# Kernel tuning notes

Hardware: AMD Instinct MI355X
Metric: run time of the kernel (lower is better)

Reference implementation:

```python
import jax, jax.numpy as jnp
import numpy as np

TOL = 1e-3


def _image_grads(F):
    # replicate-pad central difference, matches GradientBatch (conv with [-0.5,0,0.5])
    Fx = jnp.pad(F, ((0, 0), (0, 0), (0, 0), (1, 1)), mode='edge')
    gx = 0.5 * (Fx[:, :, :, 2:] - Fx[:, :, :, :-2])
    Fy = jnp.pad(F, ((0, 0), (0, 0), (1, 1), (0, 0)), mode='edge')
    gy = 0.5 * (Fy[:, :, 2:, :] - Fy[:, :, :-2, :])
    return gx, gy


def _param_to_H(p):
    B = p.shape[0]
    z = jnp.zeros((B, 1, 1), p.dtype)
    return jnp.concatenate([p, z], 1).reshape(B, 3, 3) + jnp.eye(3, dtype=p.dtype)


def _bilinear_sample(A, xw, yw):
    # grid_sample(mode='bilinear', align_corners=True, padding_mode='zeros') at pixel coords (xw, yw)
    B, k, h, w = A.shape
    x0 = jnp.floor(xw)
    y0 = jnp.floor(yw)
    fx = (xw - x0).reshape(B, 1, h * w)
    fy = (yw - y0).reshape(B, 1, h * w)
    Af = A.reshape(B, k, h * w)

    def gather(xi, yi):
        valid = (xi >= 0) & (xi <= w - 1) & (yi >= 0) & (yi <= h - 1)
        xi_c = jnp.clip(xi, 0, w - 1).astype(jnp.int32)
        yi_c = jnp.clip(yi, 0, h - 1).astype(jnp.int32)
        idx = (yi_c * w + xi_c).reshape(B, 1, h * w)
        v = jnp.take_along_axis(Af, jnp.broadcast_to(idx, (B, k, h * w)), axis=2)
        return v * valid.reshape(B, 1, h * w).astype(A.dtype)

    v00 = gather(x0, y0)
    v01 = gather(x0 + 1, y0)
    v10 = gather(x0, y0 + 1)
    v11 = gather(x0 + 1, y0 + 1)
    Q = ((1 - fx) * (1 - fy) * v00 + fx * (1 - fy) * v01
         + (1 - fx) * fy * v10 + fx * fy * v11)
    return Q.reshape(B, k, h, w)


def _deeplk(img, temp, init_param, max_itr):
    B, k, h, w = temp.shape
    dt = temp.dtype
    gx, gy = _image_grads(temp)
    # centered pixel grid (meshgrid in source: x - x.max()/2)
    x = jnp.arange(w, dtype=dt) - (w - 1) / 2.0
    y = jnp.arange(h, dtype=dt) - (h - 1) / 2.0
    X, Y = jnp.meshgrid(x, y)  # (h, w); X varies along w
    Xf = jnp.tile(X.reshape(-1), k)  # [k*h*w], tiled per channel
    Yf = jnp.tile(Y.reshape(-1), k)
    gxf = gx.reshape(B, k * h * w)
    gyf = gy.reshape(B, k * h * w)
    dIdp = jnp.stack([
        Xf * gxf, Yf * gxf, gxf,
        Xf * gyf, Yf * gyf, gyf,
        -Xf * Xf * gxf - Xf * Yf * gyf,
        -Xf * Yf * gxf - Yf * Yf * gyf,
    ], axis=2)  # [B, k*h*w, 8]
    Hmat = jnp.einsum('bnp,bnq->bpq', dIdp, dIdp)  # [B,8,8]
    invH = jnp.linalg.inv(Hmat)
    invH_dIdp = jnp.einsum('bpq,bnq->bpn', invH, dIdp)  # [B,8,k*h*w]
    xy = jnp.stack([X.reshape(-1), Y.reshape(-1), jnp.ones((h * w,), dt)], 0)  # [3, h*w]
    tolf = jnp.asarray(TOL, dt)

    def step(carry, _):
        p, dp = carry
        Hm = _param_to_H(p)
        xyw = jnp.einsum('bij,jn->bin', Hm, xy)  # [B,3,h*w]
        Xw = (xyw[:, 0] / xyw[:, 2]).reshape(B, h, w) + (w - 1) / 2.0
        Yw = (xyw[:, 1] / xyw[:, 2]).reshape(B, h, w) + (h - 1) / 2.0
        Fi_warp = _bilinear_sample(img, Xw, Yw)
        xn = Xw / ((w - 1) / 2.0) - 1.0
        yn = Yw / ((h - 1) / 2.0) - 1.0
        mask = ((xn > -1 + 2.0 / w) & (xn < 1 - 2.0 / w)
                & (yn > -1 + 2.0 / h) & (yn < 1 - 2.0 / h)).astype(dt)
        r = (Fi_warp - temp * mask[:, None]).reshape(B, k * h * w, 1)
        dp_new = jnp.einsum('bpn,bnj->bpj', invH_dIdp, r)  # [B,8,1]
        dp_new = dp_new.at[:, 6:8, 0].set(0.0)  # zero projective terms
        active = (jnp.linalg.norm(dp, axis=1, keepdims=True) > tolf).astype(dt)
        dp2 = active * dp_new  # converged samples freeze (dp stays 0)
        return (p - dp2, dp2), None

    dp0 = jnp.ones((B, 8, 1), dt)
    (p, _), _ = jax.lax.scan(step, (init_param, dp0), None, length=max_itr)
    return p


def setup_inputs() -> dict:
    key = jax.random.key(0)
    k1, k2 = jax.random.split(key)
    B, k, h, w = 8, 8, 256, 256
    img = jax.random.normal(k1, (B, k, h, w), dtype=jnp.float32)
    temp = jax.random.normal(k2, (B, k, h, w), dtype=jnp.float32)
    init_param = jnp.zeros((B, 8, 1), dtype=jnp.float32)
    return {"img": img, "temp": temp, "init_param": init_param, "max_itr": 10}


def reference(img, temp, init_param, max_itr):
    p = _deeplk(img, temp, init_param, max_itr)
    return (p, _param_to_H(p))
```

## Files before the change

kernel.cpp:

```cpp
#include <hip/hip_runtime.h>
#include <hip/hip_bf16.h>

#define B_ 8
#define K_ 8
#define H_ 256
#define W_ 256
#define HW (H_*W_)

__device__ __forceinline__ unsigned short f2bf(float f) {
    __hip_bfloat16 h = __float2bfloat16(f);
    return *reinterpret_cast<unsigned short*>(&h);
}
__device__ __forceinline__ void ub8(uint4 u, float* o) {
    o[0] = __uint_as_float(u.x << 16); o[1] = __uint_as_float(u.x & 0xffff0000u);
    o[2] = __uint_as_float(u.y << 16); o[3] = __uint_as_float(u.y & 0xffff0000u);
    o[4] = __uint_as_float(u.z << 16); o[5] = __uint_as_float(u.z & 0xffff0000u);
    o[6] = __uint_as_float(u.w << 16); o[7] = __uint_as_float(u.w & 0xffff0000u);
}
__device__ __forceinline__ float half_reduce(float v) {
    v += __shfl_down(v, 16, 64);
    v += __shfl_down(v, 8, 64);
    v += __shfl_down(v, 4, 64);
    v += __shfl_down(v, 2, 64);
    v += __shfl_down(v, 1, 64);
    return v;
}

__device__ __forceinline__ void pixel_accum(
    const uint4* __restrict__ imgT, const uint4* __restrict__ TG,
    int b, int x, int y,
    float h00, float h01, float h02, float h10, float h11, float h12,
    float h20, float h21, float* aa) {
    const int px = (y << 8) | x;
    const float X = (float)x - 127.5f, Y = (float)y - 127.5f;
    const float zw = h20 * X + h21 * Y + 1.f;
    const float Xw = (h00 * X + h01 * Y + h02) / zw + 127.5f;
    const float Yw = (h10 * X + h11 * Y + h12) / zw + 127.5f;
    const float NLO = -1.f + 2.f / 256.f, NHI = 1.f - 2.f / 256.f;
    const float xn = Xw / 127.5f - 1.f, yn = Yw / 127.5f - 1.f;
    const float m = (xn > NLO && xn < NHI && yn > NLO && yn < NHI) ? 1.f : 0.f;

    const float x0f = floorf(Xw), y0f = floorf(Yw);
    const float fx = Xw - x0f, fy = Yw - y0f;
    const float x1f = x0f + 1.f, y1f = y0f + 1.f;
    const bool vx0 = (x0f >= 0.f) && (x0f <= 255.f);
    const bool vx1 = (x1f >= 0.f) && (x1f <= 255.f);
    const bool vy0 = (y0f >= 0.f) && (y0f <= 255.f);
    const bool vy1 = (y1f >= 0.f) && (y1f <= 255.f);
    const int xi0 = (int)fminf(fmaxf(x0f, 0.f), 255.f);
    const int xi1 = (int)fminf(fmaxf(x1f, 0.f), 255.f);
    const int yi0 = (int)fminf(fmaxf(y0f, 0.f), 255.f);
    const int yi1 = (int)fminf(fmaxf(y1f, 0.f), 255.f);
    const int i00 = yi0 * W_ + xi0, i01 = yi0 * W_ + xi1;
    const int i10 = yi1 * W_ + xi0, i11 = yi1 * W_ + xi1;
    const float w00 = ((vx0 && vy0) ? 1.f : 0.f) * (1.f - fx) * (1.f - fy);
    const float w01 = ((vx1 && vy0) ? 1.f : 0.f) * fx * (1.f - fy);
    const float w10 = ((vx0 && vy1) ? 1.f : 0.f) * (1.f - fx) * fy;
    const float w11 = ((vx1 && vy1) ? 1.f : 0.f) * fx * fy;

    const int base = b * HW;
    const uint4 u00 = imgT[base + i00], u01 = imgT[base + i01];
    const uint4 u10 = imgT[base + i10], u11 = imgT[base + i11];
    const uint4* tg = TG + (size_t)(base + px) * 3;
    const uint4 t0 = tg[0], g0 = tg[1], g1 = tg[2];

    float A00[8], A01[8], A10[8], A11[8], GX[8], GY[8], TV[8];
    ub8(u00, A00); ub8(u01, A01); ub8(u10, A10); ub8(u11, A11);
    ub8(t0, TV);   ub8(g0, GX);   ub8(g1, GY);

    float vx = 0.f, vy = 0.f;
    #pragma unroll
    for (int c = 0; c < 8; ++c) {
        const float Q = w00 * A00[c] + w01 * A01[c] + w10 * A10[c] + w11 * A11[c];
        const float r = Q - TV[c] * m;
        vx += GX[c] * r;
        vy += GY[c] * r;
    }
    const float t0a = X * vx, t4a = Y * vy;
    const float cc = t0a + t4a;
    aa[0] += t0a;      aa[1] += Y * vx;  aa[2] += vx;
    aa[3] += X * vy;   aa[4] += t4a;     aa[5] += vy;
    aa[6] -= X * cc;   aa[7] -= Y * cc;
}

__global__ __launch_bounds__(256) void prep_kernel(
    const float* __restrict__ img, const float* __restrict__ temp,
    uint4* __restrict__ imgT, uint4* __restrict__ TG,
    double* __restrict__ gramP) {
    __shared__ float smem[9472];
    const int b   = blockIdx.x & 7;
    const int y   = blockIdx.x >> 3;
    const int tid = threadIdx.x;
    const int ym = (y > 0) ? y - 1 : 0;
    const int yp = (y < 255) ? y + 1 : 255;

    #pragma unroll
    for (int j = 0; j < 8; ++j) {
        const int slot = tid + 256 * j;
        const int rowid = slot >> 6, col4 = slot & 63;
        const int c = rowid >> 2, sel = rowid & 3;
        const int sy = (sel == 0) ? ym : ((sel == 2) ? yp : y);
        const float* src = ((sel == 3) ? img : temp)
                         + ((size_t)(b * K_ + c) * HW + sy * W_ + col4 * 4);
        const float4 v = *(const float4*)src;
        *(float4*)&smem[(c * 4 + sel) * 256 + col4 * 4] = v;
    }
    __syncthreads();

    const int x = tid;
    const int px = (y << 8) | x;
    const float X = (float)x - 127.5f, Y = (float)y - 127.5f;
    const int xm = (x > 0) ? x - 1 : 0;
    const int xp = (x < 255) ? x + 1 : 255;
    float Sxx = 0.f, Sxy = 0.f, Syy = 0.f;
    unsigned int imgp[4] = {0, 0, 0, 0};
    unsigned int tgp[12];
    #pragma unroll
    for (int i = 0; i < 12; ++i) tgp[i] = 0u;
    #pragma unroll
    for (int c = 0; c < 8; ++c) {
        const float* R = &smem[c * 1024];
        const float gx = 0.5f * (R[256 + xp] - R[256 + xm]);
        const float gy = 0.5f * (R[512 + x] - R[x]);
        const float tc = R[256 + x];
        const float iv = R[768 + x];
        Sxx += gx * gx; Sxy += gx * gy; Syy += gy * gy;
        const int sh = (c & 1) * 16;
        imgp[c >> 1]     |= ((unsigned int)f2bf(iv)) << sh;
        tgp[c >> 1]      |= ((unsigned int)f2bf(tc)) << sh;
        tgp[4 + (c >> 1)]|= ((unsigned int)f2bf(gx)) << sh;
        tgp[8 + (c >> 1)]|= ((unsigned int)f2bf(gy)) << sh;
    }
    const size_t gpx = (size_t)b * HW + px;
    imgT[gpx] = make_uint4(imgp[0], imgp[1], imgp[2], imgp[3]);
    uint4* tg = TG + gpx * 3;
    tg[0] = make_uint4(tgp[0], tgp[1], tgp[2],  tgp[3]);
    tg[1] = make_uint4(tgp[4], tgp[5], tgp[6],  tgp[7]);
    tg[2] = make_uint4(tgp[8], tgp[9], tgp[10], tgp[11]);
    __syncthreads();

    {
        const float av[8] = {X, Y, 1.f, 0.f, 0.f, 0.f, -X * X, -X * Y};
        const float bv[8] = {0.f, 0.f, 0.f, X, Y, 1.f, -X * Y, -Y * Y};
        int idx = 0;
        #pragma unroll
        for (int pi = 0; pi < 8; ++pi)
            #pragma unroll
            for (int qi = pi; qi < 8; ++qi) {
                smem[tid * 37 + idx] = av[pi] * av[qi] * Sxx
                    + (av[pi] * bv[qi] + av[qi] * bv[pi]) * Sxy
                    + bv[pi] * bv[qi] * Syy;
                ++idx;
            }
    }
    __syncthreads();
    #pragma unroll
    for (int st = 128; st >= 1; st >>= 1) {
        if (tid < st) {
            #pragma unroll
            for (int e = 0; e < 36; ++e)
                smem[tid * 37 + e] += smem[(tid + st) * 37 + e];
        }
        __syncthreads();
    }
    if (tid < 36) gramP[((size_t)b * 36 + tid) * 256 + y] = (double)smem[tid];
}

__global__ void invert_kernel(const double* __restrict__ gramP,
                              double* __restrict__ invH) {
    const int b = blockIdx.x;
    const int t = threadIdx.x;
    __shared__ double G[36];
    __shared__ double A[64];
    __shared__ double Bi[64];
    if (t < 36) {
        double acc = 0.0;
        const double* gp = gramP + ((size_t)b * 36 + t) * 256;
        for (int r = 0; r < 256; ++r) acc += gp[r];
        G[t] = acc;
    }
    __syncthreads();
    const int i = t >> 3, j = t & 7;
    const int pp = min(i, j), qq = max(i, j);
    const int tri = 8 * pp - (pp * (pp - 1)) / 2 + (qq - pp);
    A[t]  = G[tri];
    Bi[t] = (i == j) ? 1.0 : 0.0;
    __syncthreads();
    for (int k = 0; k < 8; ++k) {
        const double piv = A[k * 8 + k];
        __syncthreads();
        if (i == k) { A[t] /= piv; Bi[t] /= piv; }
        __syncthreads();
        const double f  = A[i * 8 + k];
        const double ak = A[k * 8 + j];
        const double bk = Bi[k * 8 + j];
        __syncthreads();
        if (i != k) { A[t] -= f * ak; Bi[t] -= f * bk; }
        __syncthreads();
    }
    invH[b * 64 + t] = Bi[t];
}

__global__ __launch_bounds__(256) void iter_kernel(
    const uint4* __restrict__ imgT, const uint4* __restrict__ TG,
    const double* __restrict__ invH, const float* __restrict__ init_param,
    const double* __restrict__ stateR, double* __restrict__ stateW,
    const float* __restrict__ sPrev, float* __restrict__ sNext,
    const int* __restrict__ max_itr, int iter) {
    if (iter >= *max_itr) return;
    __shared__ float red[2048];
    __shared__ float s8[8];
    __shared__ double sh_pd[16];
    const int b   = blockIdx.x & 7;
    const int yb  = blockIdx.x >> 3;
    const int tid = threadIdx.x;

    if (iter == 0) {
        if (tid < 8) {
            sh_pd[tid]     = (double)init_param[b * 8 + tid];
            sh_pd[8 + tid] = 1.0;
        }
    } else {
        const float* sR = sPrev + b * 512;
        const int e = tid >> 5, l = tid & 31;
        float v = sR[e * 64 + l] + sR[e * 64 + 32 + l];
        v = half_reduce(v);
        if ((tid & 31) == 0) s8[tid >> 5] = v;
        __syncthreads();
        if (tid < 8) {
            double nrm2 = 0.0;
            #pragma unroll
            for (int k2 = 0; k2 < 8; ++k2) {
                const double d = stateR[64 + b * 8 + k2];
                nrm2 += d * d;
            }
            double dpn = 0.0;
            if (tid < 6) {
                #pragma unroll
                for (int k2 = 0; k2 < 8; ++k2)
                    dpn += invH[b * 64 + tid * 8 + k2] * (double)s8[k2];
            }
            const double dp2 = (sqrt(nrm2) > 1e-3) ? dpn : 0.0;
            sh_pd[tid]     = stateR[b * 8 + tid] - dp2;
            sh_pd[8 + tid] = dp2;
        }
    }
    __syncthreads();
    if (yb == 0 && tid < 8) {
        stateW[b * 8 + tid]      = sh_pd[tid];
        stateW[64 + b * 8 + tid] = sh_pd[8 + tid];
    }

    const float h00 = 1.f + (float)sh_pd[0], h01 = (float)sh_pd[1], h02 = (float)sh_pd[2];
    const float h10 = (float)sh_pd[3], h11 = 1.f + (float)sh_pd[4], h12 = (float)sh_pd[5];
    const float h20 = (float)sh_pd[6], h21 = (float)sh_pd[7];

    float aa[8];
    #pragma unroll
    for (int e = 0; e < 8; ++e) aa[e] = 0.f;
    #pragma unroll 1
    for (int sub = 0; sub < 4; ++sub) {
        pixel_accum(imgT, TG, b, tid, yb * 4 + sub,
                    h00, h01, h02, h10, h11, h12, h20, h21, aa);
    }

    #pragma unroll
    for (int e = 0; e < 8; ++e) red[e * 256 + tid] = aa[e];
    __syncthreads();
    {
        const int e = tid >> 5, l = tid & 31;
        float v = 0.f;
        #pragma unroll
        for (int j = 0; j < 8; ++j) v += red[e * 256 + l + 32 * j];
        v = half_reduce(v);
        if ((tid & 31) == 0) sNext[b * 512 + e * 64 + yb] = v;
    }
}

__global__ void output_kernel(const double* __restrict__ invH,
                              const float* __restrict__ init_param,
                              const double* __restrict__ st0,
                              const double* __restrict__ st1,
                              const float* __restrict__ sP0,
                              const float* __restrict__ sP1,
                              const int* __restrict__ max_itr,
                              float* __restrict__ out) {
    const int tid = threadIdx.x;
    const int mi_raw = *max_itr;
    const int mi = (mi_raw > 10) ? 10 : mi_raw;
    if (mi <= 0) {
        if (tid < 64) out[tid] = init_param[tid];
        if (tid < 72) {
            const int b = tid / 9, j = tid % 9;
            float v = (j < 8) ? init_param[b * 8 + j] : 0.f;
            if (j == 0 || j == 4 || j == 8) v += 1.f;
            out[64 + tid] = v;
        }
        return;
    }
    const int pr = (mi - 1) & 1;
    const double* st = pr ? st1 : st0;
    const float*  sP = pr ? sP1 : sP0;
    __shared__ float s8[8];
    __shared__ float sh_pf[8];
    for (int b = 0; b < B_; ++b) {
        const float* sb = sP + b * 512;
        const int e = tid >> 5, l = tid & 31;
        float v = sb[e * 64 + l] + sb[e * 64 + 32 + l];
        v = half_reduce(v);
        if ((tid & 31) == 0) s8[tid >> 5] = v;
        __syncthreads();
        if (tid < 8) {
            double nrm2 = 0.0;
            #pragma unroll
            for (int k2 = 0; k2 < 8; ++k2) {
                const double d = st[64 + b * 8 + k2];
                nrm2 += d * d;
            }
            double dpn = 0.0;
            if (tid < 6) {
                #pragma unroll
                for (int k2 = 0; k2 < 8; ++k2)
                    dpn += invH[b * 64 + tid * 8 + k2] * (double)s8[k2];
            }
            const double dp2 = (sqrt(nrm2) > 1e-3) ? dpn : 0.0;
            const float pf = (float)(st[b * 8 + tid] - dp2);
            sh_pf[tid] = pf;
            out[b * 8 + tid] = pf;
        }
        __syncthreads();
        if (tid < 9) {
            float v2 = (tid < 8) ? sh_pf[tid] : 0.f;
            if (tid == 0 || tid == 4 || tid == 8) v2 += 1.f;
            out[64 + b * 9 + tid] = v2;
        }
        __syncthreads();
    }
}

extern "C" void kernel_launch(void* const* d_in, const int* in_sizes, int n_in,
                              void* d_out, int out_size, void* d_ws, size_t ws_size,
                              hipStream_t stream) {
    const float* img        = (const float*)d_in[0];
    const float* temp       = (const float*)d_in[1];
    const float* init_param = (const float*)d_in[2];
    const int*   max_itr    = (const int*)d_in[3];
    float* out = (float*)d_out;

    char* w = (char*)d_ws;
    double* gramP = (double*)w;
    double* st0   = gramP + 73728;
    double* st1   = st0 + 128;
    double* invH  = st1 + 128;
    float*  sP0   = (float*)(invH + 512);
    float*  sP1   = sP0 + 4096;
    uint4* imgT   = (uint4*)(w + 1048576);
    uint4* TG     = (uint4*)(w + 1048576 + 8388608);

    prep_kernel<<<B_ * H_, 256, 0, stream>>>(img, temp, imgT, TG, gramP);
    invert_kernel<<<B_, 64, 0, stream>>>(gramP, invH);
    for (int it = 0; it < 10; ++it) {
        const double* stR = (it & 1) ? st0 : st1;
        double*       stW = (it & 1) ? st1 : st0;
        const float*  sR  = (it & 1) ? sP0 : sP1;
        float*        sW  = (it & 1) ? sP1 : sP0;
        iter_kernel<<<512, 256, 0, stream>>>(imgT, TG, invH, init_param,
                                             stR, stW, sR, sW, max_itr, it);
    }
    output_kernel<<<1, 256, 0, stream>>>(invH, init_param, st0, st1,
                                         sP0, sP1, max_itr, out);
}
```

Baseline: 183.2 us.

## Fuse iteration kernels into one persistent kernel with per-batch atomic barriers

Replaces the ten per-iteration launches and the output kernel with a single persistent kernel of 512 blocks. Blocks of each batch sum their partial gradients with float atomics and spin-wait on a per-iteration counter before updating the parameters locally. This removes launch gaps and the global-memory state ping-pong. In exchange it needs all 512 blocks co-resident (launch bounds of 2 blocks per CU) or it deadlocks, and float atomic summation order becomes nondeterministic.

Result: slower. 320.5 us (+74.9%).

```diff
diff --git a/kernel.cpp b/kernel.cpp
--- a/kernel.cpp
+++ b/kernel.cpp
@@ -6,6 +6,7 @@
 #define H_ 256
 #define W_ 256
 #define HW (H_*W_)
+#define MAXIT 16
 
 __device__ __forceinline__ unsigned short f2bf(float f) {
     __hip_bfloat16 h = __float2bfloat16(f);
@@ -167,9 +168,13 @@
 }
 
 __global__ void invert_kernel(const double* __restrict__ gramP,
-                              double* __restrict__ invH) {
+                              double* __restrict__ invH,
+                              float* __restrict__ sg, int* __restrict__ cnt) {
     const int b = blockIdx.x;
     const int t = threadIdx.x;
+    for (int it = (t >> 3); it < MAXIT; it += 8) sg[it * 64 + b * 8 + (t & 7)] = 0.f;
+    if (t < MAXIT) cnt[t * 8 + b] = 0;
+
     __shared__ double G[36];
     __shared__ double A[64];
     __shared__ double Bi[64];
@@ -201,140 +206,99 @@
     invH[b * 64 + t] = Bi[t];
 }
 
-__global__ __launch_bounds__(256) void iter_kernel(
+__global__ __launch_bounds__(256, 2) void persist_kernel(
     const uint4* __restrict__ imgT, const uint4* __restrict__ TG,
     const double* __restrict__ invH, const float* __restrict__ init_param,
-    const double* __restrict__ stateR, double* __restrict__ stateW,
-    const float* __restrict__ sPrev, float* __restrict__ sNext,
-    const int* __restrict__ max_itr, int iter) {
-    if (iter >= *max_itr) return;
+    const int* __restrict__ max_itr,
+    float* __restrict__ sg, int* __restrict__ cnt,
+    float* __restrict__ out) {
     __shared__ float red[2048];
     __shared__ float s8[8];
+    __shared__ double sh_invH[64];
     __shared__ double sh_pd[16];
     const int b   = blockIdx.x & 7;
     const int yb  = blockIdx.x >> 3;
     const int tid = threadIdx.x;
 
-    if (iter == 0) {
-        if (tid < 8) {
-            sh_pd[tid]     = (double)init_param[b * 8 + tid];
-            sh_pd[8 + tid] = 1.0;
-        }
-    } else {
-        const float* sR = sPrev + b * 512;
-        const int e = tid >> 5, l = tid & 31;
-        float v = sR[e * 64 + l] + sR[e * 64 + 32 + l];
-        v = half_reduce(v);
-        if ((tid & 31) == 0) s8[tid >> 5] = v;
-        __syncthreads();
+    if (tid < 64) sh_invH[tid] = invH[b * 64 + tid];
+    if (tid < 8) {
+        sh_pd[tid]     = (double)init_param[b * 8 + tid];
+        sh_pd[8 + tid] = 1.0;
+    }
+    int mi = *max_itr;
+    if (mi < 0) mi = 0;
+    if (mi > MAXIT) mi = MAXIT;
+    __syncthreads();
+
+    for (int it = 0; it < mi; ++it) {
+        const float h00 = 1.f + (float)sh_pd[0], h01 = (float)sh_pd[1], h02 = (float)sh_pd[2];
+        const float h10 = (float)sh_pd[3], h11 = 1.f + (float)sh_pd[4], h12 = (float)sh_pd[5];
+        const float h20 = (float)sh_pd[6], h21 = (float)sh_pd[7];
+
+        float aa[8];
+        #pragma unroll
+        for (int e = 0; e < 8; ++e) aa[e] = 0.f;
+        #pragma unroll 1
+        for (int sub = 0; sub < 4; ++sub) {
+            pixel_accum(imgT, TG, b, tid, yb * 4 + sub,
+                        h00, h01, h02, h10, h11, h12, h20, h21, aa);
+        }
+
+        #pragma unroll
+        for (int e = 0; e < 8; ++e) red[e * 256 + tid] = aa[e];
+        __syncthreads();
+        {
+            const int e = tid >> 5, l = tid & 31;
+            float v = 0.f;
+            #pragma unroll
+            for (int j = 0; j < 8; ++j) v += red[e * 256 + l + 32 * j];
+            v = half_reduce(v);
+            if ((tid & 31) == 0) s8[e] = v;
+        }
+        __syncthreads();
+
+        float* sgo = sg + it * 64 + b * 8;
+        if (tid < 8) atomicAdd(&sgo[tid], s8[tid]);
+        __syncthreads();
+        if (tid == 0) {
+            int* cp = &cnt[it * 8 + b];
+            __hip_atomic_fetch_add(cp, 1, __ATOMIC_RELEASE, __HIP_MEMORY_SCOPE_AGENT);
+            while (__hip_atomic_load(cp, __ATOMIC_RELAXED, __HIP_MEMORY_SCOPE_AGENT) < 64)
+                __builtin_amdgcn_s_sleep(2);
+        }
+        __syncthreads();
+
+        if (tid < 8)
+            s8[tid] = __hip_atomic_load(&sgo[tid], __ATOMIC_RELAXED,
+                                        __HIP_MEMORY_SCOPE_AGENT);
+        __syncthreads();
+
         if (tid < 8) {
             double nrm2 = 0.0;
             #pragma unroll
             for (int k2 = 0; k2 < 8; ++k2) {
-                const double d = stateR[64 + b * 8 + k2];
+                const double d = sh_pd[8 + k2];
                 nrm2 += d * d;
             }
             double dpn = 0.0;
             if (tid < 6) {
                 #pragma unroll
                 for (int k2 = 0; k2 < 8; ++k2)
-                    dpn += invH[b * 64 + tid * 8 + k2] * (double)s8[k2];
+                    dpn += sh_invH[tid * 8 + k2] * (double)s8[k2];
             }
             const double dp2 = (sqrt(nrm2) > 1e-3) ? dpn : 0.0;
-            sh_pd[tid]     = stateR[b * 8 + tid] - dp2;
+            sh_pd[tid]     = sh_pd[tid] - dp2;
             sh_pd[8 + tid] = dp2;
         }
-    }
-    __syncthreads();
-    if (yb == 0 && tid < 8) {
-        stateW[b * 8 + tid]      = sh_pd[tid];
-        stateW[64 + b * 8 + tid] = sh_pd[8 + tid];
-    }
-
-    const float h00 = 1.f + (float)sh_pd[0], h01 = (float)sh_pd[1], h02 = (float)sh_pd[2];
-    const float h10 = (float)sh_pd[3], h11 = 1.f + (float)sh_pd[4], h12 = (float)sh_pd[5];
-    const float h20 = (float)sh_pd[6], h21 = (float)sh_pd[7];
-
-    float aa[8];
-    #pragma unroll
-    for (int e = 0; e < 8; ++e) aa[e] = 0.f;
-    #pragma unroll 1
-    for (int sub = 0; sub < 4; ++sub) {
-        pixel_accum(imgT, TG, b, tid, yb * 4 + sub,
-                    h00, h01, h02, h10, h11, h12, h20, h21, aa);
-    }
-
-    #pragma unroll
-    for (int e = 0; e < 8; ++e) red[e * 256 + tid] = aa[e];
-    __syncthreads();
-    {
-        const int e = tid >> 5, l = tid & 31;
-        float v = 0.f;
-        #pragma unroll
-        for (int j = 0; j < 8; ++j) v += red[e * 256 + l + 32 * j];
-        v = half_reduce(v);
-        if ((tid & 31) == 0) sNext[b * 512 + e * 64 + yb] = v;
-    }
-}
-
-__global__ void output_kernel(const double* __restrict__ invH,
-                              const float* __restrict__ init_param,
-                              const double* __restrict__ st0,
-                              const double* __restrict__ st1,
-                              const float* __restrict__ sP0,
-                              const float* __restrict__ sP1,
-                              const int* __restrict__ max_itr,
-                              float* __restrict__ out) {
-    const int tid = threadIdx.x;
-    const int mi_raw = *max_itr;
-    const int mi = (mi_raw > 10) ? 10 : mi_raw;
-    if (mi <= 0) {
-        if (tid < 64) out[tid] = init_param[tid];
-        if (tid < 72) {
-            const int b = tid / 9, j = tid % 9;
-            float v = (j < 8) ? init_param[b * 8 + j] : 0.f;
-            if (j == 0 || j == 4 || j == 8) v += 1.f;
-            out[64 + tid] = v;
-        }
-        return;
-    }
-    const int pr = (mi - 1) & 1;
-    const double* st = pr ? st1 : st0;
-    const float*  sP = pr ? sP1 : sP0;
-    __shared__ float s8[8];
-    __shared__ float sh_pf[8];
-    for (int b = 0; b < B_; ++b) {
-        const float* sb = sP + b * 512;
-        const int e = tid >> 5, l = tid & 31;
-        float v = sb[e * 64 + l] + sb[e * 64 + 32 + l];
-        v = half_reduce(v);
-        if ((tid & 31) == 0) s8[tid >> 5] = v;
-        __syncthreads();
-        if (tid < 8) {
-            double nrm2 = 0.0;
-            #pragma unroll
-            for (int k2 = 0; k2 < 8; ++k2) {
-                const double d = st[64 + b * 8 + k2];
-                nrm2 += d * d;
-            }
-            double dpn = 0.0;
-            if (tid < 6) {
-                #pragma unroll
-                for (int k2 = 0; k2 < 8; ++k2)
-                    dpn += invH[b * 64 + tid * 8 + k2] * (double)s8[k2];
-            }
-            const double dp2 = (sqrt(nrm2) > 1e-3) ? dpn : 0.0;
-            const float pf = (float)(st[b * 8 + tid] - dp2);
-            sh_pf[tid] = pf;
-            out[b * 8 + tid] = pf;
-        }
-        __syncthreads();
-        if (tid < 9) {
-            float v2 = (tid < 8) ? sh_pf[tid] : 0.f;
-            if (tid == 0 || tid == 4 || tid == 8) v2 += 1.f;
-            out[64 + b * 9 + tid] = v2;
-        }
-        __syncthreads();
+        __syncthreads();
+    }
+
+    if (yb != 0) return;
+    if (tid < 8) out[b * 8 + tid] = (float)sh_pd[tid];
+    if (tid < 9) {
+        float v = (tid < 8) ? (float)sh_pd[tid] : 0.f;
+        if (tid == 0 || tid == 4 || tid == 8) v += 1.f;
+        out[64 + b * 9 + tid] = v;
     }
 }
 
@@ -349,24 +313,14 @@
 
     char* w = (char*)d_ws;
     double* gramP = (double*)w;
-    double* st0   = gramP + 73728;
-    double* st1   = st0 + 128;
-    double* invH  = st1 + 128;
-    float*  sP0   = (float*)(invH + 512);
-    float*  sP1   = sP0 + 4096;
+    double* invH  = gramP + 73728;
+    float*  sg    = (float*)(invH + 512);
+    int*    cnt   = (int*)(sg + MAXIT * 64);
     uint4* imgT   = (uint4*)(w + 1048576);
     uint4* TG     = (uint4*)(w + 1048576 + 8388608);
 
     prep_kernel<<<B_ * H_, 256, 0, stream>>>(img, temp, imgT, TG, gramP);
-    invert_kernel<<<B_, 64, 0, stream>>>(gramP, invH);
-    for (int it = 0; it < 10; ++it) {
-        const double* stR = (it & 1) ? st0 : st1;
-        double*       stW = (it & 1) ? st1 : st0;
-        const float*  sR  = (it & 1) ? sP0 : sP1;
-        float*        sW  = (it & 1) ? sP1 : sP0;
-        iter_kernel<<<512, 256, 0, stream>>>(imgT, TG, invH, init_param,
-                                             stR, stW, sR, sW, max_itr, it);
-    }
-    output_kernel<<<1, 256, 0, stream>>>(invH, init_param, st0, st1,
-                                         sP0, sP1, max_itr, out);
-}
+    invert_kernel<<<B_, 64, 0, stream>>>(gramP, invH, sg, cnt);
+    persist_kernel<<<512, 256, 0, stream>>>(imgT, TG, invH, init_param,
+                                            max_itr, sg, cnt, out);
+}
```
